# Kernel tuning notes

Measured on AMD Instinct MI355X. Metric: run time of the kernel, lower is better.

## Reference

```python
import jax, jax.numpy as jnp
import numpy as np

EPS = 1.55e-5  # tf.math.l2_normalize epsilon semantics: x / sqrt(max(sum(x^2), eps))


def _l2norm_tokens(t):
    # normalize over the token axis (-2), matching tf.math.l2_normalize(axis=-2)
    sq = jnp.sum(t * t, axis=-2, keepdims=True)
    return t * jax.lax.rsqrt(jnp.maximum(sq, EPS))


def setup_inputs() -> dict:
    key = jax.random.key(0)
    ks = jax.random.split(key, 4)
    B, H, W, C = 16, 64, 64, 512
    heads = 8
    return {
        "x": jax.random.normal(ks[0], (B, H, W, C), jnp.float32),
        "qkv_w": jax.random.normal(ks[1], (C, 3 * C), jnp.float32) * (C ** -0.5),
        "q_bias": jnp.zeros((C,), jnp.float32),
        "v_bias": jnp.zeros((C,), jnp.float32),
        "scale": jnp.ones((heads, 1, 1), jnp.float32),
        "proj_w": jax.random.normal(ks[2], (C, C), jnp.float32) * (C ** -0.5),
        "proj_b": jnp.zeros((C,), jnp.float32),
    }


def reference(x, qkv_w, q_bias, v_bias, scale, proj_w, proj_b):
    B, H, W, C = x.shape
    heads = scale.shape[0]
    d = C // heads
    N = H * W

    # 1x1 conv QKV (no conv bias) + concatenated [q_bias, 0, v_bias]
    qkv = jnp.einsum("bhwc,cf->bhwf", x, qkv_w)
    qkv = qkv + jnp.concatenate([q_bias, jnp.zeros_like(q_bias), v_bias])
    # [B, N, heads, 3, d] -> [B, heads, N, 3, d]
    qkv = qkv.reshape(B, N, heads, 3, d).transpose(0, 2, 1, 3, 4)
    q, k, v = qkv[..., 0, :], qkv[..., 1, :], qkv[..., 2, :]  # each [B, heads, N, d]

    q = _l2norm_tokens(q)
    k = _l2norm_tokens(k)

    # channel-attention: [B, heads, d, d]
    attn = jnp.einsum("bhnd,bhne->bhde", q * jnp.exp(scale), k)
    attn = jax.nn.softmax(attn, axis=-1)

    # matmul(attn, v^T) -> [B, heads, d, N]; perm [0,3,1,2] -> [B, N, heads, d]
    out = jnp.einsum("bhde,bhne->bhdn", attn, v)
    out = out.transpose(0, 3, 1, 2).reshape(B, H, W, C)

    # output 1x1 conv projection with bias
    return jnp.einsum("bhwc,cf->bhwf", out, proj_w) + proj_b
```

## Files before the change

### kernel.cpp

```cpp
#include <hip/hip_runtime.h>
#include <stdint.h>
#include <stddef.h>

#define BATCH  16
#define HEADS  8
#define NTOK   4096
#define CDIM   512
#define FDIM   1536

typedef short bf16x8 __attribute__((ext_vector_type(8)));
typedef float fx4    __attribute__((ext_vector_type(4)));

__device__ __forceinline__ uint16_t f2bf(float f) {
    uint32_t u = __float_as_uint(f);
    return (uint16_t)((u + 0x7FFFu + ((u >> 16) & 1u)) >> 16);
}
__device__ __forceinline__ float bf2f(uint16_t u) {
    return __uint_as_float(((uint32_t)u) << 16);
}
__device__ __forceinline__ void gload16(const uint16_t* g, uint16_t* l) {
    __builtin_amdgcn_global_load_lds(
        (const __attribute__((address_space(1))) uint32_t*)(g),
        (__attribute__((address_space(3))) uint32_t*)(l), 16, 0, 0);
}

__global__ void prep_kernel(const float* __restrict__ X,
                            const float* __restrict__ qkv_w,
                            const float* __restrict__ proj_w,
                            uint16_t* __restrict__ Xb,
                            uint16_t* __restrict__ Wt, uint16_t* __restrict__ Pt,
                            float* __restrict__ Sqk) {
    const int tid = blockIdx.x * blockDim.x + threadIdx.x;
    const int stride = gridDim.x * blockDim.x;
    for (int i = tid; i < (1 << 22); i += stride) {
        const fx4* src = reinterpret_cast<const fx4*>(X + (size_t)i * 8);
        fx4 v0 = src[0], v1 = src[1];
        union { bf16x8 v; uint16_t u[8]; } pk;
        #pragma unroll
        for (int e = 0; e < 4; e++) { pk.u[e] = f2bf(v0[e]); pk.u[4 + e] = f2bf(v1[e]); }
        reinterpret_cast<bf16x8*>(Xb)[i] = pk.v;
    }
    for (int i = tid; i < FDIM * CDIM; i += stride) {
        int f = i >> 9, c = i & 511;
        Wt[i] = f2bf(qkv_w[(size_t)c * FDIM + f]);
    }
    for (int i = tid; i < CDIM * CDIM; i += stride) {
        int f = i >> 9, c = i & 511;
        Pt[i] = f2bf(proj_w[(size_t)c * CDIM + f]);
    }
    for (int i = tid; i < 16384; i += stride) Sqk[i] = 0.0f;
}

__global__ __launch_bounds__(256) void gemm_qkv_kernel(
        const uint16_t* __restrict__ Xb, const uint16_t* __restrict__ Wt,
        const float* __restrict__ q_bias, const float* __restrict__ v_bias,
        uint16_t* __restrict__ qkv) {
    __shared__ uint16_t As[128 * 64];
    __shared__ uint16_t Bs[128 * 64];
    const int bx = blockIdx.x;
    const int swz = (bx & 7) * 768 + (bx >> 3);
    const int tm = swz / 12, tn = swz % 12;
    const int gm = tm * 128, gn = tn * 128;
    const int t = threadIdx.x, lane = t & 63, w = t >> 6;
    const int wm = w >> 1, wn = w & 1;
    const int l15 = lane & 15, lg = lane >> 4;
    fx4 acc[4][4] = {};
    const int srow = t >> 3;
    const int scol = (t & 7) * 8;
    for (int k0 = 0; k0 < 512; k0 += 64) {
        const uint16_t* ga = Xb + (size_t)(gm + srow) * 512 + k0 + scol;
        const uint16_t* gb = Wt + (size_t)(gn + srow) * 512 + k0 + scol;
        uint16_t* la = &As[t * 8];
        uint16_t* lb = &Bs[t * 8];
        #pragma unroll
        for (int j = 0; j < 4; j++) {
            gload16(ga + (size_t)j * 32 * 512, la + j * 2048);
            gload16(gb + (size_t)j * 32 * 512, lb + j * 2048);
        }
        __syncthreads();
        #pragma unroll
        for (int ks = 0; ks < 2; ks++) {
            const int kof = ks * 32 + lg * 8;
            bf16x8 af[4], bfr[4];
            #pragma unroll
            for (int m = 0; m < 4; m++)
                af[m] = *reinterpret_cast<const bf16x8*>(&As[(wm * 64 + m * 16 + l15) * 64 + kof]);
            #pragma unroll
            for (int n = 0; n < 4; n++)
                bfr[n] = *reinterpret_cast<const bf16x8*>(&Bs[(wn * 64 + n * 16 + l15) * 64 + kof]);
            #pragma unroll
            for (int m = 0; m < 4; m++)
                #pragma unroll
                for (int n = 0; n < 4; n++)
                    acc[m][n] = __builtin_amdgcn_mfma_f32_16x16x32_bf16(
                        af[m], bfr[n], acc[m][n], 0, 0, 0);
        }
        __syncthreads();
    }
    #pragma unroll
    for (int m = 0; m < 4; m++) {
        #pragma unroll
        for (int n = 0; n < 4; n++) {
            const int col = gn + wn * 64 + n * 16 + l15;
            const float bias = (col < 512) ? q_bias[col]
                              : ((col < 1024) ? 0.0f : v_bias[col - 1024]);
            #pragma unroll
            for (int r = 0; r < 4; r++) {
                const int row = gm + wm * 64 + m * 16 + lg * 4 + r;
                qkv[(size_t)row * FDIM + col] = f2bf(acc[m][n][r] + bias);
            }
        }
    }
}

__global__ __launch_bounds__(256) void attn_qk_kernel(
        const uint16_t* __restrict__ qkv, float* __restrict__ Gpart,
        float* __restrict__ Sq, float* __restrict__ Sk) {
    const int blk = blockIdx.x;
    const int bh = blk >> 2, quarter = blk & 3;
    const int b = bh >> 3, h = bh & 7;
    const int t = threadIdx.x, lane = t & 63, w = t >> 6;
    const int l15 = lane & 15, lg = lane >> 4;
    const int wr = w >> 1, wc = w & 1;
    __shared__ uint16_t qT[64][72];
    __shared__ uint16_t kT[64][72];
    const int tok = t >> 2, chgrp = t & 3, ch0 = chgrp * 16;
    const uint16_t* base = qkv + (size_t)b * NTOK * FDIM + h * 192;
    fx4 acc[2][2] = {};
    float sq[16] = {}, sk[16] = {};
    for (int tile = 0; tile < 16; tile++) {
        const int n = quarter * 1024 + tile * 64 + tok;
        const uint16_t* row = base + (size_t)n * FDIM;
        union { bf16x8 v; uint16_t u[8]; } qa, qb, ka, kb;
        qa.v = *reinterpret_cast<const bf16x8*>(row + ch0);
        qb.v = *reinterpret_cast<const bf16x8*>(row + ch0 + 8);
        ka.v = *reinterpret_cast<const bf16x8*>(row + 64 + ch0);
        kb.v = *reinterpret_cast<const bf16x8*>(row + 64 + ch0 + 8);
        __syncthreads();
        #pragma unroll
        for (int j = 0; j < 8; j++) {
            qT[ch0 + j][tok] = qa.u[j];
            qT[ch0 + 8 + j][tok] = qb.u[j];
            kT[ch0 + j][tok] = ka.u[j];
            kT[ch0 + 8 + j][tok] = kb.u[j];
            float f0 = bf2f(qa.u[j]), f1 = bf2f(qb.u[j]);
            float g0 = bf2f(ka.u[j]), g1 = bf2f(kb.u[j]);
            sq[j] += f0 * f0; sq[8 + j] += f1 * f1;
            sk[j] += g0 * g0; sk[8 + j] += g1 * g1;
        }
        __syncthreads();
        #pragma unroll
        for (int ks = 0; ks < 2; ks++) {
            const int kof = ks * 32 + lg * 8;
            bf16x8 a0 = *reinterpret_cast<const bf16x8*>(&qT[wr * 32 + l15][kof]);
            bf16x8 a1 = *reinterpret_cast<const bf16x8*>(&qT[wr * 32 + 16 + l15][kof]);
            bf16x8 b0 = *reinterpret_cast<const bf16x8*>(&kT[wc * 32 + l15][kof]);
            bf16x8 b1 = *reinterpret_cast<const bf16x8*>(&kT[wc * 32 + 16 + l15][kof]);
            acc[0][0] = __builtin_amdgcn_mfma_f32_16x16x32_bf16(a0, b0, acc[0][0], 0, 0, 0);
            acc[0][1] = __builtin_amdgcn_mfma_f32_16x16x32_bf16(a0, b1, acc[0][1], 0, 0, 0);
            acc[1][0] = __builtin_amdgcn_mfma_f32_16x16x32_bf16(a1, b0, acc[1][0], 0, 0, 0);
            acc[1][1] = __builtin_amdgcn_mfma_f32_16x16x32_bf16(a1, b1, acc[1][1], 0, 0, 0);
        }
    }
    #pragma unroll
    for (int off = 4; off <= 32; off <<= 1) {
        #pragma unroll
        for (int j = 0; j < 16; j++) {
            sq[j] += __shfl_xor(sq[j], off, 64);
            sk[j] += __shfl_xor(sk[j], off, 64);
        }
    }
    if (lane < 4) {
        #pragma unroll
        for (int j = 0; j < 16; j++) {
            atomicAdd(&Sq[bh * 64 + lane * 16 + j], sq[j]);
            atomicAdd(&Sk[bh * 64 + lane * 16 + j], sk[j]);
        }
    }
    float* gp = Gpart + (size_t)quarter * 524288 + (size_t)bh * 4096;
    #pragma unroll
    for (int mi = 0; mi < 2; mi++)
        #pragma unroll
        for (int ni = 0; ni < 2; ni++)
            #pragma unroll
            for (int r = 0; r < 4; r++) {
                const int d = wr * 32 + mi * 16 + lg * 4 + r;
                const int e = wc * 32 + ni * 16 + l15;
                gp[d * 64 + e] = acc[mi][ni][r];
            }
}

__global__ void attn_finalize_kernel(const float* __restrict__ Gpart,
                                     const float* __restrict__ Sq,
                                     const float* __restrict__ Sk,
                                     const float* __restrict__ scale,
                                     uint16_t* __restrict__ attnb) {
    const int bh = blockIdx.x;
    const int h = bh & 7;
    const int t = threadIdx.x;
    const int e = t & 63, w = t >> 6;
    const float es = expf(scale[h]);
    const float rk = rsqrtf(fmaxf(Sk[bh * 64 + e], 1.55e-5f));
    const float* g0 = Gpart + (size_t)bh * 4096;
    for (int d = w; d < 64; d += 4) {
        const float rq = rsqrtf(fmaxf(Sq[bh * 64 + d], 1.55e-5f));
        float g = g0[d * 64 + e] + g0[524288 + d * 64 + e]
                + g0[1048576 + d * 64 + e] + g0[1572864 + d * 64 + e];
        float x = es * g * rq * rk;
        float m = x;
        #pragma unroll
        for (int off = 32; off; off >>= 1) m = fmaxf(m, __shfl_xor(m, off, 64));
        float p = expf(x - m);
        float s = p;
        #pragma unroll
        for (int off = 32; off; off >>= 1) s += __shfl_xor(s, off, 64);
        attnb[(size_t)bh * 4096 + d * 64 + e] = f2bf(p / s);
    }
}

__global__ __launch_bounds__(256) void pv_kernel(
        const uint16_t* __restrict__ qkv, const uint16_t* __restrict__ attnb,
        uint16_t* __restrict__ out_t) {
    const int blk = blockIdx.x;
    const int bh = blk >> 6, chunk = blk & 63;
    const int b = bh >> 3, h = bh & 7;
    const int n0 = chunk * 64;
    const int t = threadIdx.x, lane = t & 63, w = t >> 6;
    const int l15 = lane & 15, lg = lane >> 4;
    __shared__ uint16_t Vs[64][72];
    {
        const int tok = t >> 2, seg = (t & 3) * 16;
        const uint16_t* vrow = qkv + (size_t)(b * NTOK + n0 + tok) * FDIM + h * 192 + 128 + seg;
        *reinterpret_cast<bf16x8*>(&Vs[tok][seg])     = *reinterpret_cast<const bf16x8*>(vrow);
        *reinterpret_cast<bf16x8*>(&Vs[tok][seg + 8]) = *reinterpret_cast<const bf16x8*>(vrow + 8);
    }
    bf16x8 bfr[4][2];
    const uint16_t* ab = attnb + (size_t)bh * 4096;
    #pragma unroll
    for (int n = 0; n < 4; n++)
        #pragma unroll
        for (int ks = 0; ks < 2; ks++)
            bfr[n][ks] = *reinterpret_cast<const bf16x8*>(ab + (n * 16 + l15) * 64 + ks * 32 + lg * 8);
    __syncthreads();
    fx4 acc[4] = {};
    #pragma unroll
    for (int ks = 0; ks < 2; ks++) {
        const int kof = ks * 32 + lg * 8;
        bf16x8 a = *reinterpret_cast<const bf16x8*>(&Vs[w * 16 + l15][kof]);
        #pragma unroll
        for (int n = 0; n < 4; n++)
            acc[n] = __builtin_amdgcn_mfma_f32_16x16x32_bf16(a, bfr[n][ks], acc[n], 0, 0, 0);
    }
    #pragma unroll
    for (int n = 0; n < 4; n++)
        #pragma unroll
        for (int r = 0; r < 4; r++) {
            const int tokg = b * NTOK + n0 + w * 16 + lg * 4 + r;
            out_t[(size_t)tokg * CDIM + h * 64 + n * 16 + l15] = f2bf(acc[n][r]);
        }
}

__global__ __launch_bounds__(256) void gemm_proj_kernel(
        const uint16_t* __restrict__ At, const uint16_t* __restrict__ Pt,
        const float* __restrict__ proj_b, float* __restrict__ outp) {
    __shared__ uint16_t As[128 * 64];
    __shared__ uint16_t Bs[128 * 64];
    const int bx = blockIdx.x;
    const int swz = (bx & 7) * 256 + (bx >> 3);
    const int tn = swz & 3, tm = swz >> 2;
    const int gm = tm * 128, gn = tn * 128;
    const int t = threadIdx.x, lane = t & 63, w = t >> 6;
    const int wm = w >> 1, wn = w & 1;
    const int l15 = lane & 15, lg = lane >> 4;
    fx4 acc[4][4] = {};
    const int srow = t >> 3;
    const int scol = (t & 7) * 8;
    for (int k0 = 0; k0 < 512; k0 += 64) {
        const uint16_t* ga = At + (size_t)(gm + srow) * 512 + k0 + scol;
        const uint16_t* gb = Pt + (size_t)(gn + srow) * 512 + k0 + scol;
        uint16_t* la = &As[t * 8];
        uint16_t* lb = &Bs[t * 8];
        #pragma unroll
        for (int j = 0; j < 4; j++) {
            gload16(ga + (size_t)j * 32 * 512, la + j * 2048);
            gload16(gb + (size_t)j * 32 * 512, lb + j * 2048);
        }
        __syncthreads();
        #pragma unroll
        for (int ks = 0; ks < 2; ks++) {
            const int kof = ks * 32 + lg * 8;
            bf16x8 af[4], bfr[4];
            #pragma unroll
            for (int m = 0; m < 4; m++)
                af[m] = *reinterpret_cast<const bf16x8*>(&As[(wm * 64 + m * 16 + l15) * 64 + kof]);
            #pragma unroll
            for (int n = 0; n < 4; n++)
                bfr[n] = *reinterpret_cast<const bf16x8*>(&Bs[(wn * 64 + n * 16 + l15) * 64 + kof]);
            #pragma unroll
            for (int m = 0; m < 4; m++)
                #pragma unroll
                for (int n = 0; n < 4; n++)
                    acc[m][n] = __builtin_amdgcn_mfma_f32_16x16x32_bf16(
                        af[m], bfr[n], acc[m][n], 0, 0, 0);
        }
        __syncthreads();
    }
    #pragma unroll
    for (int m = 0; m < 4; m++) {
        #pragma unroll
        for (int n = 0; n < 4; n++) {
            const int col = gn + wn * 64 + n * 16 + l15;
            const float bias = proj_b[col];
            #pragma unroll
            for (int r = 0; r < 4; r++) {
                const int row = gm + wm * 64 + m * 16 + lg * 4 + r;
                outp[(size_t)row * CDIM + col] = acc[m][n][r] + bias;
            }
        }
    }
}

extern "C" void kernel_launch(void* const* d_in, const int* in_sizes, int n_in,
                              void* d_out, int out_size, void* d_ws, size_t ws_size,
                              hipStream_t stream) {
    (void)in_sizes; (void)n_in; (void)out_size; (void)ws_size;
    const float* x      = (const float*)d_in[0];
    const float* qkv_w  = (const float*)d_in[1];
    const float* q_bias = (const float*)d_in[2];
    const float* v_bias = (const float*)d_in[3];
    const float* scale  = (const float*)d_in[4];
    const float* proj_w = (const float*)d_in[5];
    const float* proj_b = (const float*)d_in[6];
    float* out = (float*)d_out;

    char* wsp = (char*)d_ws;
    uint16_t* Wt    = (uint16_t*)(wsp);
    uint16_t* Pt    = (uint16_t*)(wsp + 1572864);
    float*    Sq    = (float*)   (wsp + 2097152);
    float*    Sk    = (float*)   (wsp + 2129920);
    float*    Gpart = (float*)   (wsp + 2162688);
    uint16_t* attnb = (uint16_t*)(wsp + 10551296);
    uint16_t* qkv   = (uint16_t*)(wsp + 11599872);
    uint16_t* Xb    = (uint16_t*)(wsp + 212926464);
    uint16_t* out_t = Xb;

    hipLaunchKernelGGL(prep_kernel, dim3(2048), dim3(256), 0, stream,
                       x, qkv_w, proj_w, Xb, Wt, Pt, Sq);
    hipLaunchKernelGGL(gemm_qkv_kernel, dim3(6144), dim3(256), 0, stream,
                       Xb, Wt, q_bias, v_bias, qkv);
    hipLaunchKernelGGL(attn_qk_kernel, dim3(512), dim3(256), 0, stream,
                       qkv, Gpart, Sq, Sk);
    hipLaunchKernelGGL(attn_finalize_kernel, dim3(128), dim3(256), 0, stream,
                       Gpart, Sq, Sk, scale, attnb);
    hipLaunchKernelGGL(pv_kernel, dim3(8192), dim3(256), 0, stream,
                       qkv, attnb, out_t);
    hipLaunchKernelGGL(gemm_proj_kernel, dim3(2048), dim3(256), 0, stream,
                       out_t, Pt, proj_b, out);
}
```

Measured before the change: 633.1 us.

## Emit Q/K transposed from QKV GEMM epilogue, swizzle LDS, tiled weight transpose

The QKV GEMM epilogue stages its output tile in shared memory, then writes Q and K transposed per head (d-major over tokens) and V per token/head. It also accumulates the squared norms with atomics, so attn_qk can stream Q/K with direct global-to-LDS loads instead of transposing in registers. LDS tiles across the GEMMs, attn_qk and pv use an XOR swizzle to avoid bank conflicts. Weight transposition moves to a tiled shared-memory kernel for coalesced access. This adds an extra kernel launch, more atomics, and a heavier epilogue in the large GEMM.

```diff
diff --git a/kernel.cpp b/kernel.cpp
--- a/kernel.cpp
+++ b/kernel.cpp
@@ -23,12 +23,37 @@
         (const __attribute__((address_space(1))) uint32_t*)(g),
         (__attribute__((address_space(3))) uint32_t*)(l), 16, 0, 0);
 }
+__device__ __forceinline__ int cidx(int row, int col) {
+    return row * 128 + (col ^ ((row & 7) << 3));
+}
+
+__global__ void transpose_w_kernel(const float* __restrict__ qkv_w,
+                                   const float* __restrict__ proj_w,
+                                   uint16_t* __restrict__ Wt,
+                                   uint16_t* __restrict__ Pt) {
+    __shared__ uint16_t tile[32][33];
+    int blk = blockIdx.x;
+    const float* src; uint16_t* dst; int W, Hh, r0, c0;
+    if (blk < 768) {
+        int tr = blk / 48, tc = blk % 48;
+        src = qkv_w; dst = Wt; W = 1536; Hh = 512; r0 = tr * 32; c0 = tc * 32;
+    } else {
+        blk -= 768;
+        int tr = blk / 16, tc = blk % 16;
+        src = proj_w; dst = Pt; W = 512; Hh = 512; r0 = tr * 32; c0 = tc * 32;
+    }
+    const int tx = threadIdx.x & 31, ty = threadIdx.x >> 5;
+    #pragma unroll
+    for (int j = 0; j < 4; j++)
+        tile[ty + 8 * j][tx] = f2bf(src[(size_t)(r0 + ty + 8 * j) * W + c0 + tx]);
+    __syncthreads();
+    #pragma unroll
+    for (int j = 0; j < 4; j++)
+        dst[(size_t)(c0 + ty + 8 * j) * Hh + r0 + tx] = tile[tx][ty + 8 * j];
+}
 
 __global__ void prep_kernel(const float* __restrict__ X,
-                            const float* __restrict__ qkv_w,
-                            const float* __restrict__ proj_w,
                             uint16_t* __restrict__ Xb,
-                            uint16_t* __restrict__ Wt, uint16_t* __restrict__ Pt,
                             float* __restrict__ Sqk) {
     const int tid = blockIdx.x * blockDim.x + threadIdx.x;
     const int stride = gridDim.x * blockDim.x;
@@ -40,36 +65,32 @@
         for (int e = 0; e < 4; e++) { pk.u[e] = f2bf(v0[e]); pk.u[4 + e] = f2bf(v1[e]); }
         reinterpret_cast<bf16x8*>(Xb)[i] = pk.v;
     }
-    for (int i = tid; i < FDIM * CDIM; i += stride) {
-        int f = i >> 9, c = i & 511;
-        Wt[i] = f2bf(qkv_w[(size_t)c * FDIM + f]);
-    }
-    for (int i = tid; i < CDIM * CDIM; i += stride) {
-        int f = i >> 9, c = i & 511;
-        Pt[i] = f2bf(proj_w[(size_t)c * CDIM + f]);
-    }
     for (int i = tid; i < 16384; i += stride) Sqk[i] = 0.0f;
 }
 
 __global__ __launch_bounds__(256) void gemm_qkv_kernel(
         const uint16_t* __restrict__ Xb, const uint16_t* __restrict__ Wt,
         const float* __restrict__ q_bias, const float* __restrict__ v_bias,
-        uint16_t* __restrict__ qkv) {
-    __shared__ uint16_t As[128 * 64];
-    __shared__ uint16_t Bs[128 * 64];
+        uint16_t* __restrict__ QT, uint16_t* __restrict__ KT,
+        uint16_t* __restrict__ VT,
+        float* __restrict__ Sq, float* __restrict__ Sk) {
+    __shared__ uint16_t sh[128 * 128];
+    uint16_t* As = sh;
+    uint16_t* Bs = sh + 8192;
     const int bx = blockIdx.x;
     const int swz = (bx & 7) * 768 + (bx >> 3);
     const int tm = swz / 12, tn = swz % 12;
     const int gm = tm * 128, gn = tn * 128;
+    const int b = gm >> 12, tok0 = gm & 4095;
     const int t = threadIdx.x, lane = t & 63, w = t >> 6;
     const int wm = w >> 1, wn = w & 1;
     const int l15 = lane & 15, lg = lane >> 4;
     fx4 acc[4][4] = {};
-    const int srow = t >> 3;
-    const int scol = (t & 7) * 8;
+    const int skey = (t >> 3) & 7;
+    const int scol0 = ((t & 7) ^ skey) * 8;
     for (int k0 = 0; k0 < 512; k0 += 64) {
-        const uint16_t* ga = Xb + (size_t)(gm + srow) * 512 + k0 + scol;
-        const uint16_t* gb = Wt + (size_t)(gn + srow) * 512 + k0 + scol;
+        const uint16_t* ga = Xb + (size_t)(gm + (t >> 3)) * 512 + k0 + scol0;
+        const uint16_t* gb = Wt + (size_t)(gn + (t >> 3)) * 512 + k0 + scol0;
         uint16_t* la = &As[t * 8];
         uint16_t* lb = &Bs[t * 8];
         #pragma unroll
@@ -83,11 +104,15 @@
             const int kof = ks * 32 + lg * 8;
             bf16x8 af[4], bfr[4];
             #pragma unroll
-            for (int m = 0; m < 4; m++)
-                af[m] = *reinterpret_cast<const bf16x8*>(&As[(wm * 64 + m * 16 + l15) * 64 + kof]);
-            #pragma unroll
-            for (int n = 0; n < 4; n++)
-                bfr[n] = *reinterpret_cast<const bf16x8*>(&Bs[(wn * 64 + n * 16 + l15) * 64 + kof]);
+            for (int m = 0; m < 4; m++) {
+                const int row = wm * 64 + m * 16 + l15;
+                af[m] = *reinterpret_cast<const bf16x8*>(&As[row * 64 + (kof ^ ((row & 7) << 3))]);
+            }
+            #pragma unroll
+            for (int n = 0; n < 4; n++) {
+                const int row = wn * 64 + n * 16 + l15;
+                bfr[n] = *reinterpret_cast<const bf16x8*>(&Bs[row * 64 + (kof ^ ((row & 7) << 3))]);
+            }
             #pragma unroll
             for (int m = 0; m < 4; m++)
                 #pragma unroll
@@ -98,84 +123,92 @@
         __syncthreads();
     }
     #pragma unroll
-    for (int m = 0; m < 4; m++) {
-        #pragma unroll
-        for (int n = 0; n < 4; n++) {
-            const int col = gn + wn * 64 + n * 16 + l15;
-            const float bias = (col < 512) ? q_bias[col]
-                              : ((col < 1024) ? 0.0f : v_bias[col - 1024]);
+    for (int n = 0; n < 4; n++) {
+        const int col = gn + wn * 64 + n * 16 + l15;
+        const float bias = (col < 512) ? q_bias[col]
+                          : ((col < 1024) ? 0.0f : v_bias[col - 1024]);
+        #pragma unroll
+        for (int m = 0; m < 4; m++)
             #pragma unroll
             for (int r = 0; r < 4; r++) {
-                const int row = gm + wm * 64 + m * 16 + lg * 4 + r;
-                qkv[(size_t)row * FDIM + col] = f2bf(acc[m][n][r] + bias);
-            }
+                const int lrow = wm * 64 + m * 16 + lg * 4 + r;
+                const int lcol = wn * 64 + n * 16 + l15;
+                sh[cidx(lrow, lcol)] = f2bf(acc[m][n][r] + bias);
+            }
+    }
+    __syncthreads();
+    const int cc = t >> 7, tloc = t & 127;
+    const int u = (gn >> 6) + cc;
+    const int h = u / 3, which = u % 3;
+    const int bh = b * 8 + h;
+    if (which < 2) {
+        const int d = tloc & 63, oct = tloc >> 6;
+        uint16_t* dst = (which == 0 ? QT : KT)
+                        + ((size_t)bh * 64 + d) * 4096 + tok0 + oct * 64;
+        float ss = 0.f;
+        #pragma unroll
+        for (int g = 0; g < 8; g++) {
+            union { bf16x8 v; uint16_t u16v[8]; } pk;
+            #pragma unroll
+            for (int s2 = 0; s2 < 8; s2++) {
+                uint16_t val = sh[cidx(oct * 64 + g * 8 + s2, cc * 64 + d)];
+                pk.u16v[s2] = val;
+                float f = bf2f(val);
+                ss += f * f;
+            }
+            *reinterpret_cast<bf16x8*>(dst + g * 8) = pk.v;
+        }
+        atomicAdd((which == 0 ? Sq : Sk) + bh * 64 + d, ss);
+    } else {
+        const int tok = tloc;
+        uint16_t* dst = VT + (size_t)(gm + tok) * 512 + h * 64;
+        #pragma unroll
+        for (int bb = 0; bb < 8; bb++) {
+            bf16x8 v = *reinterpret_cast<const bf16x8*>(&sh[cidx(tok, cc * 64 + bb * 8)]);
+            *reinterpret_cast<bf16x8*>(dst + bb * 8) = v;
         }
     }
 }
 
 __global__ __launch_bounds__(256) void attn_qk_kernel(
-        const uint16_t* __restrict__ qkv, float* __restrict__ Gpart,
-        float* __restrict__ Sq, float* __restrict__ Sk) {
+        const uint16_t* __restrict__ QT, const uint16_t* __restrict__ KT,
+        float* __restrict__ Gpart) {
+    __shared__ uint16_t Qs[64 * 128];
+    __shared__ uint16_t Ks[64 * 128];
     const int blk = blockIdx.x;
     const int bh = blk >> 2, quarter = blk & 3;
-    const int b = bh >> 3, h = bh & 7;
     const int t = threadIdx.x, lane = t & 63, w = t >> 6;
     const int l15 = lane & 15, lg = lane >> 4;
     const int wr = w >> 1, wc = w & 1;
-    __shared__ uint16_t qT[64][72];
-    __shared__ uint16_t kT[64][72];
-    const int tok = t >> 2, chgrp = t & 3, ch0 = chgrp * 16;
-    const uint16_t* base = qkv + (size_t)b * NTOK * FDIM + h * 192;
     fx4 acc[2][2] = {};
-    float sq[16] = {}, sk[16] = {};
-    for (int tile = 0; tile < 16; tile++) {
-        const int n = quarter * 1024 + tile * 64 + tok;
-        const uint16_t* row = base + (size_t)n * FDIM;
-        union { bf16x8 v; uint16_t u[8]; } qa, qb, ka, kb;
-        qa.v = *reinterpret_cast<const bf16x8*>(row + ch0);
-        qb.v = *reinterpret_cast<const bf16x8*>(row + ch0 + 8);
-        ka.v = *reinterpret_cast<const bf16x8*>(row + 64 + ch0);
-        kb.v = *reinterpret_cast<const bf16x8*>(row + 64 + ch0 + 8);
-        __syncthreads();
-        #pragma unroll
-        for (int j = 0; j < 8; j++) {
-            qT[ch0 + j][tok] = qa.u[j];
-            qT[ch0 + 8 + j][tok] = qb.u[j];
-            kT[ch0 + j][tok] = ka.u[j];
-            kT[ch0 + 8 + j][tok] = kb.u[j];
-            float f0 = bf2f(qa.u[j]), f1 = bf2f(qb.u[j]);
-            float g0 = bf2f(ka.u[j]), g1 = bf2f(kb.u[j]);
-            sq[j] += f0 * f0; sq[8 + j] += f1 * f1;
-            sk[j] += g0 * g0; sk[8 + j] += g1 * g1;
-        }
-        __syncthreads();
-        #pragma unroll
-        for (int ks = 0; ks < 2; ks++) {
+    const uint16_t* qbase = QT + (size_t)bh * 64 * 4096;
+    const uint16_t* kbase = KT + (size_t)bh * 64 * 4096;
+    for (int it = 0; it < 8; it++) {
+        const int tokt = quarter * 1024 + it * 128;
+        #pragma unroll
+        for (int j = 0; j < 4; j++) {
+            const int li = j * 256 + t;
+            const int row = li >> 4;
+            const int src_off = (((li & 15) ^ (row & 7)) << 3);
+            gload16(qbase + (size_t)row * 4096 + tokt + src_off, &Qs[li * 8]);
+            gload16(kbase + (size_t)row * 4096 + tokt + src_off, &Ks[li * 8]);
+        }
+        __syncthreads();
+        #pragma unroll
+        for (int ks = 0; ks < 4; ks++) {
             const int kof = ks * 32 + lg * 8;
-            bf16x8 a0 = *reinterpret_cast<const bf16x8*>(&qT[wr * 32 + l15][kof]);
-            bf16x8 a1 = *reinterpret_cast<const bf16x8*>(&qT[wr * 32 + 16 + l15][kof]);
-            bf16x8 b0 = *reinterpret_cast<const bf16x8*>(&kT[wc * 32 + l15][kof]);
-            bf16x8 b1 = *reinterpret_cast<const bf16x8*>(&kT[wc * 32 + 16 + l15][kof]);
+            const int ra0 = wr * 32 + l15,      ra1 = wr * 32 + 16 + l15;
+            const int rb0 = wc * 32 + l15,      rb1 = wc * 32 + 16 + l15;
+            bf16x8 a0 = *reinterpret_cast<const bf16x8*>(&Qs[ra0 * 128 + (kof ^ ((ra0 & 7) << 3))]);
+            bf16x8 a1 = *reinterpret_cast<const bf16x8*>(&Qs[ra1 * 128 + (kof ^ ((ra1 & 7) << 3))]);
+            bf16x8 b0 = *reinterpret_cast<const bf16x8*>(&Ks[rb0 * 128 + (kof ^ ((rb0 & 7) << 3))]);
+            bf16x8 b1 = *reinterpret_cast<const bf16x8*>(&Ks[rb1 * 128 + (kof ^ ((rb1 & 7) << 3))]);
             acc[0][0] = __builtin_amdgcn_mfma_f32_16x16x32_bf16(a0, b0, acc[0][0], 0, 0, 0);
             acc[0][1] = __builtin_amdgcn_mfma_f32_16x16x32_bf16(a0, b1, acc[0][1], 0, 0, 0);
             acc[1][0] = __builtin_amdgcn_mfma_f32_16x16x32_bf16(a1, b0, acc[1][0], 0, 0, 0);
             acc[1][1] = __builtin_amdgcn_mfma_f32_16x16x32_bf16(a1, b1, acc[1][1], 0, 0, 0);
         }
-    }
-    #pragma unroll
-    for (int off = 4; off <= 32; off <<= 1) {
-        #pragma unroll
-        for (int j = 0; j < 16; j++) {
-            sq[j] += __shfl_xor(sq[j], off, 64);
-            sk[j] += __shfl_xor(sk[j], off, 64);
-        }
-    }
-    if (lane < 4) {
-        #pragma unroll
-        for (int j = 0; j < 16; j++) {
-            atomicAdd(&Sq[bh * 64 + lane * 16 + j], sq[j]);
-            atomicAdd(&Sk[bh * 64 + lane * 16 + j], sk[j]);
-        }
+        __syncthreads();
     }
     float* gp = Gpart + (size_t)quarter * 524288 + (size_t)bh * 4096;
     #pragma unroll
@@ -219,20 +252,21 @@
 }
 
 __global__ __launch_bounds__(256) void pv_kernel(
-        const uint16_t* __restrict__ qkv, const uint16_t* __restrict__ attnb,
+        const uint16_t* __restrict__ VT, const uint16_t* __restrict__ attnb,
         uint16_t* __restrict__ out_t) {
+    __shared__ uint16_t Vs[64 * 64];
     const int blk = blockIdx.x;
     const int bh = blk >> 6, chunk = blk & 63;
     const int b = bh >> 3, h = bh & 7;
     const int n0 = chunk * 64;
     const int t = threadIdx.x, lane = t & 63, w = t >> 6;
     const int l15 = lane & 15, lg = lane >> 4;
-    __shared__ uint16_t Vs[64][72];
-    {
-        const int tok = t >> 2, seg = (t & 3) * 16;
-        const uint16_t* vrow = qkv + (size_t)(b * NTOK + n0 + tok) * FDIM + h * 192 + 128 + seg;
-        *reinterpret_cast<bf16x8*>(&Vs[tok][seg])     = *reinterpret_cast<const bf16x8*>(vrow);
-        *reinterpret_cast<bf16x8*>(&Vs[tok][seg + 8]) = *reinterpret_cast<const bf16x8*>(vrow + 8);
+    #pragma unroll
+    for (int j = 0; j < 2; j++) {
+        const int li = j * 256 + t;
+        const int row = li >> 3;
+        const int src_off = (((li & 7) ^ (row & 7)) << 3);
+        gload16(VT + (size_t)(b * NTOK + n0 + row) * 512 + h * 64 + src_off, &Vs[li * 8]);
     }
     bf16x8 bfr[4][2];
     const uint16_t* ab = attnb + (size_t)bh * 4096;
@@ -245,8 +279,9 @@
     fx4 acc[4] = {};
     #pragma unroll
     for (int ks = 0; ks < 2; ks++) {
+        const int row = w * 16 + l15;
         const int kof = ks * 32 + lg * 8;
-        bf16x8 a = *reinterpret_cast<const bf16x8*>(&Vs[w * 16 + l15][kof]);
+        bf16x8 a = *reinterpret_cast<const bf16x8*>(&Vs[row * 64 + (kof ^ ((row & 7) << 3))]);
         #pragma unroll
         for (int n = 0; n < 4; n++)
             acc[n] = __builtin_amdgcn_mfma_f32_16x16x32_bf16(a, bfr[n][ks], acc[n], 0, 0, 0);
@@ -273,17 +308,15 @@
     const int wm = w >> 1, wn = w & 1;
     const int l15 = lane & 15, lg = lane >> 4;
     fx4 acc[4][4] = {};
-    const int srow = t >> 3;
-    const int scol = (t & 7) * 8;
+    const int skey = (t >> 3) & 7;
+    const int scol0 = ((t & 7) ^ skey) * 8;
     for (int k0 = 0; k0 < 512; k0 += 64) {
-        const uint16_t* ga = At + (size_t)(gm + srow) * 512 + k0 + scol;
-        const uint16_t* gb = Pt + (size_t)(gn + srow) * 512 + k0 + scol;
-        uint16_t* la = &As[t * 8];
-        uint16_t* lb = &Bs[t * 8];
+        const uint16_t* ga = At + (size_t)(gm + (t >> 3)) * 512 + k0 + scol0;
+        const uint16_t* gb = Pt + (size_t)(gn + (t >> 3)) * 512 + k0 + scol0;
         #pragma unroll
         for (int j = 0; j < 4; j++) {
-            gload16(ga + (size_t)j * 32 * 512, la + j * 2048);
-            gload16(gb + (size_t)j * 32 * 512, lb + j * 2048);
+            gload16(ga + (size_t)j * 32 * 512, &As[t * 8 + j * 2048]);
+            gload16(gb + (size_t)j * 32 * 512, &Bs[t * 8 + j * 2048]);
         }
         __syncthreads();
         #pragma unroll
@@ -291,11 +324,15 @@
             const int kof = ks * 32 + lg * 8;
             bf16x8 af[4], bfr[4];
             #pragma unroll
-            for (int m = 0; m < 4; m++)
-                af[m] = *reinterpret_cast<const bf16x8*>(&As[(wm * 64 + m * 16 + l15) * 64 + kof]);
-            #pragma unroll
-            for (int n = 0; n < 4; n++)
-                bfr[n] = *reinterpret_cast<const bf16x8*>(&Bs[(wn * 64 + n * 16 + l15) * 64 + kof]);
+            for (int m = 0; m < 4; m++) {
+                const int row = wm * 64 + m * 16 + l15;
+                af[m] = *reinterpret_cast<const bf16x8*>(&As[row * 64 + (kof ^ ((row & 7) << 3))]);
+            }
+            #pragma unroll
+            for (int n = 0; n < 4; n++) {
+                const int row = wn * 64 + n * 16 + l15;
+                bfr[n] = *reinterpret_cast<const bf16x8*>(&Bs[row * 64 + (kof ^ ((row & 7) << 3))]);
+            }
             #pragma unroll
             for (int m = 0; m < 4; m++)
                 #pragma unroll
@@ -340,20 +377,24 @@
     float*    Sk    = (float*)   (wsp + 2129920);
     float*    Gpart = (float*)   (wsp + 2162688);
     uint16_t* attnb = (uint16_t*)(wsp + 10551296);
-    uint16_t* qkv   = (uint16_t*)(wsp + 11599872);
+    uint16_t* QT    = (uint16_t*)(wsp + 11599872);
+    uint16_t* KT    = (uint16_t*)(wsp + 78708736);
+    uint16_t* VT    = (uint16_t*)(wsp + 145817600);
     uint16_t* Xb    = (uint16_t*)(wsp + 212926464);
     uint16_t* out_t = Xb;
 
+    hipLaunchKernelGGL(transpose_w_kernel, dim3(1024), dim3(256), 0, stream,
+                       qkv_w, proj_w, Wt, Pt);
     hipLaunchKernelGGL(prep_kernel, dim3(2048), dim3(256), 0, stream,
-                       x, qkv_w, proj_w, Xb, Wt, Pt, Sq);
+                       x, Xb, Sq);
     hipLaunchKernelGGL(gemm_qkv_kernel, dim3(6144), dim3(256), 0, stream,
-                       Xb, Wt, q_bias, v_bias, qkv);
+                       Xb, Wt, q_bias, v_bias, QT, KT, VT, Sq, Sk);
     hipLaunchKernelGGL(attn_qk_kernel, dim3(512), dim3(256), 0, stream,
-                       qkv, Gpart, Sq, Sk);
+                       QT, KT, Gpart);
     hipLaunchKernelGGL(attn_finalize_kernel, dim3(128), dim3(256), 0, stream,
                        Gpart, Sq, Sk, scale, attnb);
     hipLaunchKernelGGL(pv_kernel, dim3(8192), dim3(256), 0, stream,
-                       qkv, attnb, out_t);
+                       VT, attnb, out_t);
     hipLaunchKernelGGL(gemm_proj_kernel, dim3(2048), dim3(256), 0, stream,
                        out_t, Pt, proj_b, out);
 }
```

Result: faster. 578.5 us (-8.6%).
